# Kernel tuning notes

Measured on AMD Instinct MI355X. Metric: run time of the kernel, lower is better.

Reference implementation:

```python
import jax, jax.numpy as jnp
import numpy as np

D_IN = 4096
D_OUT = 4096
EPS_NORM = 1e-6
EPS_Q = 1e-8


def _ternary_quantize(w):
    # per-output-channel absmean scale, then round/clamp to {-1,0,1}
    gamma = jnp.mean(jnp.abs(w), axis=-1)
    w_q = jnp.clip(jnp.round(w / (gamma[:, None] + EPS_Q)), -1.0, 1.0)
    return w_q, gamma


def setup_inputs() -> dict:
    key = jax.random.key(0)
    kx, kw = jax.random.split(key)
    x = jax.random.normal(kx, (2, 4096, D_IN), dtype=jnp.float32)
    # kaiming-uniform-like init then ternarize (mirrors torch __init__)
    bound = 1.0 / np.sqrt(D_IN)
    w_init = jax.random.uniform(kw, (D_OUT, D_IN), minval=-bound, maxval=bound, dtype=jnp.float32)
    w_q, gamma = _ternary_quantize(w_init)
    norm_weight = jnp.ones((D_IN,), dtype=jnp.float32)
    return {"x": x, "norm_weight": norm_weight, "w_q": w_q, "gamma": gamma}


def reference(x, norm_weight, w_q, gamma):
    # RMSNorm
    rms = jnp.sqrt(jnp.mean(x * x, axis=-1, keepdims=True) + EPS_NORM)
    xn = x / rms * norm_weight
    # ternary linear (dense fp32 GEMM, math identical to F.linear) + per-channel scale
    y = jnp.einsum('bsd,od->bso', xn, w_q) * gamma
    return y
```

## Files before the change

### kernel.cpp

```cpp
#include <hip/hip_runtime.h>
#include <hip/hip_bf16.h>
#include <stdint.h>

#define D_IN  4096
#define D_OUT 4096
#define MROWS 8192

using i32x4 = __attribute__((ext_vector_type(4))) int;

__global__ __launch_bounds__(256) void prep_kernel(
    const float* __restrict__ x, const float* __restrict__ nw,
    signed char* __restrict__ xq, float* __restrict__ srow,
    const float* __restrict__ wq, signed char* __restrict__ wb) {
  const int b = blockIdx.x;
  const int t = threadIdx.x;

  if (b < 2048) {
    const int lane = t & 63;
    const int row  = b * 4 + (t >> 6);
    const float4* xr  = (const float4*)(x + (size_t)row * D_IN);
    const float4* nw4 = (const float4*)nw;

    float4 p[16];
    float ss = 0.f, mx = 0.f;
#pragma unroll
    for (int c = 0; c < 4; ++c) {
      float4 v[4], w[4];
#pragma unroll
      for (int i = 0; i < 4; ++i) {
        v[i] = xr[(c * 4 + i) * 64 + lane];
        w[i] = nw4[(c * 4 + i) * 64 + lane];
      }
#pragma unroll
      for (int i = 0; i < 4; ++i) {
        ss += v[i].x * v[i].x + v[i].y * v[i].y +
              v[i].z * v[i].z + v[i].w * v[i].w;
        float4 pp;
        pp.x = v[i].x * w[i].x; pp.y = v[i].y * w[i].y;
        pp.z = v[i].z * w[i].z; pp.w = v[i].w * w[i].w;
        p[c * 4 + i] = pp;
        mx = fmaxf(mx, fmaxf(fmaxf(fabsf(pp.x), fabsf(pp.y)),
                             fmaxf(fabsf(pp.z), fabsf(pp.w))));
      }
    }
#pragma unroll
    for (int off = 1; off < 64; off <<= 1) {
      ss += __shfl_xor(ss, off, 64);
      mx = fmaxf(mx, __shfl_xor(mx, off, 64));
    }
    const float scale  = rsqrtf(ss * (1.0f / D_IN) + 1e-6f);
    const float rowmax = mx * scale;
    const float s = fmaxf(rowmax, 1e-20f) * (1.0f / 127.0f);
    const float f = scale / s;
    if (lane == 0) srow[row] = s;

    int* out = (int*)(xq + (size_t)row * D_IN);
#pragma unroll
    for (int i = 0; i < 16; ++i) {
      const int q0 = (int)rintf(p[i].x * f);
      const int q1 = (int)rintf(p[i].y * f);
      const int q2 = (int)rintf(p[i].z * f);
      const int q3 = (int)rintf(p[i].w * f);
      out[i * 64 + lane] =
          (q0 & 0xFF) | ((q1 & 0xFF) << 8) | ((q2 & 0xFF) << 16) | (q3 << 24);
    }
  } else {
    const int cb = b - 2048;
    const float4* w4 = (const float4*)wq;
    int* o = (int*)wb;
#pragma unroll
    for (int i = 0; i < 4; ++i) {
      const int idx = cb * 1024 + i * 256 + t;
      const float4 v = w4[idx];
      const int q0 = (int)v.x, q1 = (int)v.y, q2 = (int)v.z, q3 = (int)v.w;
      o[idx] = (q0 & 0xFF) | ((q1 & 0xFF) << 8) | ((q2 & 0xFF) << 16) | (q3 << 24);
    }
  }
}

#define BM 256
#define BN 256
#define BKB 64
#define NKT (D_IN / BKB)
#define SLOT_BYTES (BM * BKB)

#define WVM(n_) asm volatile("s_waitcnt vmcnt(" #n_ ")" ::: "memory")
#define BAR()   __builtin_amdgcn_s_barrier()

#define STAGE(t_)                                                             \
  do {                                                                        \
    _Pragma("unroll") for (int _i = 0; _i < 2; ++_i)                          \
        __builtin_amdgcn_global_load_lds(                                     \
            (__attribute__((address_space(1))) void*)(A + aOff[_i] +          \
                                                      (t_) * BKB),            \
            (__attribute__((address_space(3))) void*)&sA[(t_) & 3]            \
                                                       [ldsOff[_i]],          \
            16, 0, 0);                                                        \
    _Pragma("unroll") for (int _i = 0; _i < 2; ++_i)                          \
        __builtin_amdgcn_global_load_lds(                                     \
            (__attribute__((address_space(1))) void*)(B + bOff[_i] +          \
                                                      (t_) * BKB),            \
            (__attribute__((address_space(3))) void*)&sB[(t_) & 3]            \
                                                       [ldsOff[_i]],          \
            16, 0, 0);                                                        \
  } while (0)

#define READF(t_, fa_, fb_)                                                   \
  do {                                                                        \
    _Pragma("unroll") for (int _i = 0; _i < 8; ++_i)                          \
        fa_[_i] = *(const i32x4*)&sA[(t_) & 3][aoff0 + _i * (16 * BKB)];      \
    _Pragma("unroll") for (int _j = 0; _j < 4; ++_j)                          \
        fb_[_j] = *(const i32x4*)&sB[(t_) & 3][boff0 + _j * (16 * BKB)];      \
  } while (0)

#define MFMA_C(fa_, fb_)                                                      \
  do {                                                                        \
    __builtin_amdgcn_s_setprio(1);                                            \
    _Pragma("unroll") for (int _i = 0; _i < 8; ++_i)                          \
        _Pragma("unroll") for (int _j = 0; _j < 4; ++_j)                      \
            acc[_i][_j] = __builtin_amdgcn_mfma_i32_16x16x64_i8(              \
                fa_[_i], fb_[_j], acc[_i][_j], 0, 0, 0);                      \
    __builtin_amdgcn_s_setprio(0);                                            \
  } while (0)

#define BODY_A(T_, fcA_, fcB_, fnA_, fnB_, STG_, WAIT_)                       \
  do {                                                                        \
    READF((T_) + 1, fnA_, fnB_);                                              \
    STG_;                                                                     \
    MFMA_C(fcA_, fcB_);                                                       \
    WAIT_;                                                                    \
    BAR();                                                                    \
  } while (0)

#define BODY_B(T_, fcA_, fcB_, fnA_, fnB_, STG_, WAIT_)                       \
  do {                                                                        \
    MFMA_C(fcA_, fcB_);                                                       \
    READF((T_) + 1, fnA_, fnB_);                                              \
    STG_;                                                                     \
    WAIT_;                                                                    \
    BAR();                                                                    \
  } while (0)

__global__ __launch_bounds__(512, 2) void gemm_kernel(
    const signed char* __restrict__ A,
    const signed char* __restrict__ B,
    const float* __restrict__ srow,
    const float* __restrict__ gamma,
    float* __restrict__ C) {
  __shared__ __align__(16) signed char sA[4][SLOT_BYTES];
  __shared__ __align__(16) signed char sB[4][SLOT_BYTES];

  const int tid  = threadIdx.x;
  const int lane = tid & 63;
  const int wv   = tid >> 6;
  const int wm   = wv >> 2;
  const int wn   = wv & 3;
  const int bn   = blockIdx.x;
  const int bm   = blockIdx.y;

  i32x4 acc[8][4];
#pragma unroll
  for (int i = 0; i < 8; ++i)
#pragma unroll
    for (int j = 0; j < 4; ++j) acc[i][j] = (i32x4){0, 0, 0, 0};

  size_t aOff[2], bOff[2];
  int ldsOff[2];
#pragma unroll
  for (int i = 0; i < 2; ++i) {
    const int c  = i * 512 + tid;
    const int r  = c >> 2;
    const int cc = ((c & 3) ^ ((r >> 1) & 3)) * 16;
    aOff[i] = (size_t)(bm * BM + r) * D_IN + cc;
    bOff[i] = (size_t)(bn * BN + r) * D_IN + cc;
    ldsOff[i] = (i * 512 + wv * 64) * 16;
  }

  const int kk    = (((lane >> 4) ^ ((lane >> 1) & 3))) * 16;
  const int aoff0 = (wm * 128 + (lane & 15)) * BKB + kk;
  const int boff0 = (wn * 64  + (lane & 15)) * BKB + kk;

  i32x4 f0a[8], f0b[4], f1a[8], f1b[4];

  STAGE(0); STAGE(1); STAGE(2);
  WVM(4);
  BAR();
  READF(0, f0a, f0b);

  if (wm) {
#pragma unroll 1
    for (int T = 0; T < NKT - 4; T += 2) {
      BODY_B(T,     f0a, f0b, f1a, f1b, STAGE(T + 3), WVM(4));
      BODY_B(T + 1, f1a, f1b, f0a, f0b, STAGE(T + 4), WVM(4));
    }
    BODY_B(60, f0a, f0b, f1a, f1b, STAGE(63), WVM(4));
    BODY_B(61, f1a, f1b, f0a, f0b, ,          WVM(0));
  } else {
#pragma unroll 1
    for (int T = 0; T < NKT - 4; T += 2) {
      BODY_A(T,     f0a, f0b, f1a, f1b, STAGE(T + 3), WVM(4));
      BODY_A(T + 1, f1a, f1b, f0a, f0b, STAGE(T + 4), WVM(4));
    }
    BODY_A(60, f0a, f0b, f1a, f1b, STAGE(63), WVM(4));
    BODY_A(61, f1a, f1b, f0a, f0b, ,          WVM(0));
  }
  READF(63, f1a, f1b);
  MFMA_C(f0a, f0b);
  MFMA_C(f1a, f1b);

  const int col0 = bn * BN + wn * 64 + (lane & 15);
  const int row0 = bm * BM + wm * 128 + ((lane >> 4) * 4);
  float g[4];
#pragma unroll
  for (int j = 0; j < 4; ++j) g[j] = gamma[col0 + j * 16];

#pragma unroll
  for (int i = 0; i < 8; ++i) {
#pragma unroll
    for (int r = 0; r < 4; ++r) {
      const int row = row0 + i * 16 + r;
      const float sr = srow[row];
#pragma unroll
      for (int j = 0; j < 4; ++j) {
        C[(size_t)row * D_OUT + col0 + j * 16] =
            (float)acc[i][j][r] * sr * g[j];
      }
    }
  }
}

#undef BODY_A
#undef BODY_B
#undef MFMA_C
#undef READF
#undef STAGE
#undef WVM
#undef BAR

extern "C" void kernel_launch(void* const* d_in, const int* in_sizes, int n_in,
                              void* d_out, int out_size, void* d_ws, size_t ws_size,
                              hipStream_t stream) {
  const float* x     = (const float*)d_in[0];
  const float* nw    = (const float*)d_in[1];
  const float* wq    = (const float*)d_in[2];
  const float* gamma = (const float*)d_in[3];
  float* y = (float*)d_out;

  signed char* xq = (signed char*)d_ws;
  signed char* wb = xq + (size_t)MROWS * D_IN;
  float* srow = (float*)(wb + (size_t)D_OUT * D_IN);

  prep_kernel<<<2048 + 4096, 256, 0, stream>>>(x, nw, xq, srow, wq, wb);

  gemm_kernel<<<dim3(D_OUT / BN, MROWS / BM), 512, 0, stream>>>(xq, wb, srow, gamma, y);
}
```

Before: 383.0 us.

## Shrink GEMM tile to 128x128 with 4 waves and drop split wave scheduling

Reduces the int8 GEMM block tile from 256x256 (8 waves) to 128x128 (4 waves, 64x64 per wave), cutting per-wave accumulators and fragments in half. It also removes the split where half the waves ran MFMA before LDS reads and half after, using a single read-then-compute ordering. The smaller tile gives 2048 blocks instead of 512, which may improve occupancy and tail balance. In exchange, global and LDS traffic per MFMA roughly doubles and the wave-staggered overlap is lost.

```diff
diff --git a/kernel.cpp b/kernel.cpp
--- a/kernel.cpp
+++ b/kernel.cpp
@@ -78,8 +78,8 @@
   }
 }
 
-#define BM 256
-#define BN 256
+#define BM 128
+#define BN 128
 #define BKB 64
 #define NKT (D_IN / BKB)
 #define SLOT_BYTES (BM * BKB)
@@ -107,7 +107,7 @@
 
 #define READF(t_, fa_, fb_)                                                   \
   do {                                                                        \
-    _Pragma("unroll") for (int _i = 0; _i < 8; ++_i)                          \
+    _Pragma("unroll") for (int _i = 0; _i < 4; ++_i)                          \
         fa_[_i] = *(const i32x4*)&sA[(t_) & 3][aoff0 + _i * (16 * BKB)];      \
     _Pragma("unroll") for (int _j = 0; _j < 4; ++_j)                          \
         fb_[_j] = *(const i32x4*)&sB[(t_) & 3][boff0 + _j * (16 * BKB)];      \
@@ -116,14 +116,14 @@
 #define MFMA_C(fa_, fb_)                                                      \
   do {                                                                        \
     __builtin_amdgcn_s_setprio(1);                                            \
-    _Pragma("unroll") for (int _i = 0; _i < 8; ++_i)                          \
+    _Pragma("unroll") for (int _i = 0; _i < 4; ++_i)                          \
         _Pragma("unroll") for (int _j = 0; _j < 4; ++_j)                      \
             acc[_i][_j] = __builtin_amdgcn_mfma_i32_16x16x64_i8(              \
                 fa_[_i], fb_[_j], acc[_i][_j], 0, 0, 0);                      \
     __builtin_amdgcn_s_setprio(0);                                            \
   } while (0)
 
-#define BODY_A(T_, fcA_, fcB_, fnA_, fnB_, STG_, WAIT_)                       \
+#define BODY(T_, fcA_, fcB_, fnA_, fnB_, STG_, WAIT_)                         \
   do {                                                                        \
     READF((T_) + 1, fnA_, fnB_);                                              \
     STG_;                                                                     \
@@ -132,16 +132,7 @@
     BAR();                                                                    \
   } while (0)
 
-#define BODY_B(T_, fcA_, fcB_, fnA_, fnB_, STG_, WAIT_)                       \
-  do {                                                                        \
-    MFMA_C(fcA_, fcB_);                                                       \
-    READF((T_) + 1, fnA_, fnB_);                                              \
-    STG_;                                                                     \
-    WAIT_;                                                                    \
-    BAR();                                                                    \
-  } while (0)
-
-__global__ __launch_bounds__(512, 2) void gemm_kernel(
+__global__ __launch_bounds__(256, 2) void gemm_kernel(
     const signed char* __restrict__ A,
     const signed char* __restrict__ B,
     const float* __restrict__ srow,
@@ -153,14 +144,14 @@
   const int tid  = threadIdx.x;
   const int lane = tid & 63;
   const int wv   = tid >> 6;
-  const int wm   = wv >> 2;
-  const int wn   = wv & 3;
+  const int wm   = wv >> 1;
+  const int wn   = wv & 1;
   const int bn   = blockIdx.x;
   const int bm   = blockIdx.y;
 
-  i32x4 acc[8][4];
-#pragma unroll
-  for (int i = 0; i < 8; ++i)
+  i32x4 acc[4][4];
+#pragma unroll
+  for (int i = 0; i < 4; ++i)
 #pragma unroll
     for (int j = 0; j < 4; ++j) acc[i][j] = (i32x4){0, 0, 0, 0};
 
@@ -168,54 +159,44 @@
   int ldsOff[2];
 #pragma unroll
   for (int i = 0; i < 2; ++i) {
-    const int c  = i * 512 + tid;
+    const int c  = i * 256 + tid;
     const int r  = c >> 2;
     const int cc = ((c & 3) ^ ((r >> 1) & 3)) * 16;
     aOff[i] = (size_t)(bm * BM + r) * D_IN + cc;
     bOff[i] = (size_t)(bn * BN + r) * D_IN + cc;
-    ldsOff[i] = (i * 512 + wv * 64) * 16;
+    ldsOff[i] = (i * 256 + wv * 64) * 16;
   }
 
   const int kk    = (((lane >> 4) ^ ((lane >> 1) & 3))) * 16;
-  const int aoff0 = (wm * 128 + (lane & 15)) * BKB + kk;
-  const int boff0 = (wn * 64  + (lane & 15)) * BKB + kk;
-
-  i32x4 f0a[8], f0b[4], f1a[8], f1b[4];
+  const int aoff0 = (wm * 64 + (lane & 15)) * BKB + kk;
+  const int boff0 = (wn * 64 + (lane & 15)) * BKB + kk;
+
+  i32x4 f0a[4], f0b[4], f1a[4], f1b[4];
 
   STAGE(0); STAGE(1); STAGE(2);
   WVM(4);
   BAR();
   READF(0, f0a, f0b);
 
-  if (wm) {
 #pragma unroll 1
-    for (int T = 0; T < NKT - 4; T += 2) {
-      BODY_B(T,     f0a, f0b, f1a, f1b, STAGE(T + 3), WVM(4));
-      BODY_B(T + 1, f1a, f1b, f0a, f0b, STAGE(T + 4), WVM(4));
-    }
-    BODY_B(60, f0a, f0b, f1a, f1b, STAGE(63), WVM(4));
-    BODY_B(61, f1a, f1b, f0a, f0b, ,          WVM(0));
-  } else {
-#pragma unroll 1
-    for (int T = 0; T < NKT - 4; T += 2) {
-      BODY_A(T,     f0a, f0b, f1a, f1b, STAGE(T + 3), WVM(4));
-      BODY_A(T + 1, f1a, f1b, f0a, f0b, STAGE(T + 4), WVM(4));
-    }
-    BODY_A(60, f0a, f0b, f1a, f1b, STAGE(63), WVM(4));
-    BODY_A(61, f1a, f1b, f0a, f0b, ,          WVM(0));
-  }
+  for (int T = 0; T < NKT - 4; T += 2) {
+    BODY(T,     f0a, f0b, f1a, f1b, STAGE(T + 3), WVM(4));
+    BODY(T + 1, f1a, f1b, f0a, f0b, STAGE(T + 4), WVM(4));
+  }
+  BODY(60, f0a, f0b, f1a, f1b, STAGE(63), WVM(4));
+  BODY(61, f1a, f1b, f0a, f0b, ,          WVM(0));
   READF(63, f1a, f1b);
   MFMA_C(f0a, f0b);
   MFMA_C(f1a, f1b);
 
   const int col0 = bn * BN + wn * 64 + (lane & 15);
-  const int row0 = bm * BM + wm * 128 + ((lane >> 4) * 4);
+  const int row0 = bm * BM + wm * 64 + ((lane >> 4) * 4);
   float g[4];
 #pragma unroll
   for (int j = 0; j < 4; ++j) g[j] = gamma[col0 + j * 16];
 
 #pragma unroll
-  for (int i = 0; i < 8; ++i) {
+  for (int i = 0; i < 4; ++i) {
 #pragma unroll
     for (int r = 0; r < 4; ++r) {
       const int row = row0 + i * 16 + r;
@@ -229,8 +210,7 @@
   }
 }
 
-#undef BODY_A
-#undef BODY_B
+#undef BODY
 #undef MFMA_C
 #undef READF
 #undef STAGE
@@ -252,5 +232,5 @@
 
   prep_kernel<<<2048 + 4096, 256, 0, stream>>>(x, nw, xq, srow, wq, wb);
 
-  gemm_kernel<<<dim3(D_OUT / BN, MROWS / BM), 512, 0, stream>>>(xq, wb, srow, gamma, y);
+  gemm_kernel<<<dim3(D_OUT / BN, MROWS / BM), 256, 0, stream>>>(xq, wb, srow, gamma, y);
 }
```

New measurement: 411.3 us. 7.4% more time.

## Pre-swizzle weights into MFMA fragment layout and load B directly to registers

Applied to the files above, without the earlier changes.

The weight packing step now writes int8 weights in a per-16-row tile, per-k-step fragment layout so each lane's MFMA B operand is one contiguous 16-byte chunk. The GEMM drops the LDS staging buffer for B and loads B fragments straight from global memory into registers one step ahead, keeping only A in LDS. This halves LDS use and LDS traffic and removes the split wave-scheduling variants, but B loads now go through the global/L2 path per wave without LDS sharing across waves, and the vmcnt waits were adjusted.

```diff
diff --git a/kernel.cpp b/kernel.cpp
--- a/kernel.cpp
+++ b/kernel.cpp
@@ -66,15 +66,24 @@
     }
   } else {
     const int cb = b - 2048;
-    const float4* w4 = (const float4*)wq;
-    int* o = (int*)wb;
+    const int c  = cb * 256 + t;
+    const int nt = c >> 12;
+    const int cc = c & 4095;
+    const int ks = cc >> 6;
+    const int l  = cc & 63;
+    const int row  = nt * 16 + (l & 15);
+    const int col0 = ks * 64 + (l >> 4) * 16;
+    const float4* src = (const float4*)(wq + (size_t)row * D_IN + col0);
+    int o4[4];
 #pragma unroll
     for (int i = 0; i < 4; ++i) {
-      const int idx = cb * 1024 + i * 256 + t;
-      const float4 v = w4[idx];
+      const float4 v = src[i];
       const int q0 = (int)v.x, q1 = (int)v.y, q2 = (int)v.z, q3 = (int)v.w;
-      o[idx] = (q0 & 0xFF) | ((q1 & 0xFF) << 8) | ((q2 & 0xFF) << 16) | (q3 << 24);
-    }
+      o4[i] = (q0 & 0xFF) | ((q1 & 0xFF) << 8) | ((q2 & 0xFF) << 16) |
+              (q3 << 24);
+    }
+    *(i32x4*)(wb + (size_t)nt * 65536 + ks * 1024 + l * 16) =
+        (i32x4){o4[0], o4[1], o4[2], o4[3]};
   }
 }
 
@@ -87,7 +96,7 @@
 #define WVM(n_) asm volatile("s_waitcnt vmcnt(" #n_ ")" ::: "memory")
 #define BAR()   __builtin_amdgcn_s_barrier()
 
-#define STAGE(t_)                                                             \
+#define STAGE_A(t_)                                                           \
   do {                                                                        \
     _Pragma("unroll") for (int _i = 0; _i < 2; ++_i)                          \
         __builtin_amdgcn_global_load_lds(                                     \
@@ -96,47 +105,36 @@
             (__attribute__((address_space(3))) void*)&sA[(t_) & 3]            \
                                                        [ldsOff[_i]],          \
             16, 0, 0);                                                        \
-    _Pragma("unroll") for (int _i = 0; _i < 2; ++_i)                          \
-        __builtin_amdgcn_global_load_lds(                                     \
-            (__attribute__((address_space(1))) void*)(B + bOff[_i] +          \
-                                                      (t_) * BKB),            \
-            (__attribute__((address_space(3))) void*)&sB[(t_) & 3]            \
-                                                       [ldsOff[_i]],          \
-            16, 0, 0);                                                        \
-  } while (0)
-
-#define READF(t_, fa_, fb_)                                                   \
+  } while (0)
+
+#define READF_A(t_, fa_)                                                      \
   do {                                                                        \
     _Pragma("unroll") for (int _i = 0; _i < 8; ++_i)                          \
         fa_[_i] = *(const i32x4*)&sA[(t_) & 3][aoff0 + _i * (16 * BKB)];      \
+  } while (0)
+
+#define LOADB(t_, bf_)                                                        \
+  do {                                                                        \
     _Pragma("unroll") for (int _j = 0; _j < 4; ++_j)                          \
-        fb_[_j] = *(const i32x4*)&sB[(t_) & 3][boff0 + _j * (16 * BKB)];      \
-  } while (0)
-
-#define MFMA_C(fa_, fb_)                                                      \
+        bf_[_j] = *(const i32x4*)(Bp[_j] + (size_t)(t_) * 1024);              \
+  } while (0)
+
+#define MFMA_C(fa_, bf_)                                                      \
   do {                                                                        \
     __builtin_amdgcn_s_setprio(1);                                            \
     _Pragma("unroll") for (int _i = 0; _i < 8; ++_i)                          \
         _Pragma("unroll") for (int _j = 0; _j < 4; ++_j)                      \
             acc[_i][_j] = __builtin_amdgcn_mfma_i32_16x16x64_i8(              \
-                fa_[_i], fb_[_j], acc[_i][_j], 0, 0, 0);                      \
+                fa_[_i], bf_[_j], acc[_i][_j], 0, 0, 0);                      \
     __builtin_amdgcn_s_setprio(0);                                            \
   } while (0)
 
-#define BODY_A(T_, fcA_, fcB_, fnA_, fnB_, STG_, WAIT_)                       \
-  do {                                                                        \
-    READF((T_) + 1, fnA_, fnB_);                                              \
+#define BODY(T_, fcA_, bfc_, fnA_, bfn_, STG_, WAIT_)                         \
+  do {                                                                        \
+    READF_A((T_) + 1, fnA_);                                                  \
+    LOADB((T_) + 1, bfn_);                                                    \
     STG_;                                                                     \
-    MFMA_C(fcA_, fcB_);                                                       \
-    WAIT_;                                                                    \
-    BAR();                                                                    \
-  } while (0)
-
-#define BODY_B(T_, fcA_, fcB_, fnA_, fnB_, STG_, WAIT_)                       \
-  do {                                                                        \
-    MFMA_C(fcA_, fcB_);                                                       \
-    READF((T_) + 1, fnA_, fnB_);                                              \
-    STG_;                                                                     \
+    MFMA_C(fcA_, bfc_);                                                       \
     WAIT_;                                                                    \
     BAR();                                                                    \
   } while (0)
@@ -148,7 +146,6 @@
     const float* __restrict__ gamma,
     float* __restrict__ C) {
   __shared__ __align__(16) signed char sA[4][SLOT_BYTES];
-  __shared__ __align__(16) signed char sB[4][SLOT_BYTES];
 
   const int tid  = threadIdx.x;
   const int lane = tid & 63;
@@ -164,7 +161,7 @@
 #pragma unroll
     for (int j = 0; j < 4; ++j) acc[i][j] = (i32x4){0, 0, 0, 0};
 
-  size_t aOff[2], bOff[2];
+  size_t aOff[2];
   int ldsOff[2];
 #pragma unroll
   for (int i = 0; i < 2; ++i) {
@@ -172,41 +169,36 @@
     const int r  = c >> 2;
     const int cc = ((c & 3) ^ ((r >> 1) & 3)) * 16;
     aOff[i] = (size_t)(bm * BM + r) * D_IN + cc;
-    bOff[i] = (size_t)(bn * BN + r) * D_IN + cc;
     ldsOff[i] = (i * 512 + wv * 64) * 16;
   }
 
   const int kk    = (((lane >> 4) ^ ((lane >> 1) & 3))) * 16;
   const int aoff0 = (wm * 128 + (lane & 15)) * BKB + kk;
-  const int boff0 = (wn * 64  + (lane & 15)) * BKB + kk;
-
-  i32x4 f0a[8], f0b[4], f1a[8], f1b[4];
-
-  STAGE(0); STAGE(1); STAGE(2);
-  WVM(4);
+
+  const signed char* Bp[4];
+#pragma unroll
+  for (int j = 0; j < 4; ++j)
+    Bp[j] = B + (size_t)(bn * 16 + wn * 4 + j) * 65536 + lane * 16;
+
+  i32x4 f0a[8], f1a[8], bf0[4], bf1[4];
+
+  STAGE_A(0); STAGE_A(1); STAGE_A(2);
+  LOADB(0, bf0);
+  WVM(6);
   BAR();
-  READF(0, f0a, f0b);
-
-  if (wm) {
+  READF_A(0, f0a);
+
 #pragma unroll 1
-    for (int T = 0; T < NKT - 4; T += 2) {
-      BODY_B(T,     f0a, f0b, f1a, f1b, STAGE(T + 3), WVM(4));
-      BODY_B(T + 1, f1a, f1b, f0a, f0b, STAGE(T + 4), WVM(4));
-    }
-    BODY_B(60, f0a, f0b, f1a, f1b, STAGE(63), WVM(4));
-    BODY_B(61, f1a, f1b, f0a, f0b, ,          WVM(0));
-  } else {
-#pragma unroll 1
-    for (int T = 0; T < NKT - 4; T += 2) {
-      BODY_A(T,     f0a, f0b, f1a, f1b, STAGE(T + 3), WVM(4));
-      BODY_A(T + 1, f1a, f1b, f0a, f0b, STAGE(T + 4), WVM(4));
-    }
-    BODY_A(60, f0a, f0b, f1a, f1b, STAGE(63), WVM(4));
-    BODY_A(61, f1a, f1b, f0a, f0b, ,          WVM(0));
-  }
-  READF(63, f1a, f1b);
-  MFMA_C(f0a, f0b);
-  MFMA_C(f1a, f1b);
+  for (int T = 0; T < NKT - 4; T += 2) {
+    BODY(T,     f0a, bf0, f1a, bf1, STAGE_A(T + 3), WVM(6));
+    BODY(T + 1, f1a, bf1, f0a, bf0, STAGE_A(T + 4), WVM(6));
+  }
+  BODY(60, f0a, bf0, f1a, bf1, STAGE_A(63), WVM(6));
+  BODY(61, f1a, bf1, f0a, bf0, ,            WVM(4));
+  READF_A(63, f1a);
+  LOADB(63, bf1);
+  MFMA_C(f0a, bf0);
+  MFMA_C(f1a, bf1);
 
   const int col0 = bn * BN + wn * 64 + (lane & 15);
   const int row0 = bm * BM + wm * 128 + ((lane >> 4) * 4);
@@ -229,11 +221,11 @@
   }
 }
 
-#undef BODY_A
-#undef BODY_B
+#undef BODY
 #undef MFMA_C
-#undef READF
-#undef STAGE
+#undef LOADB
+#undef READF_A
+#undef STAGE_A
 #undef WVM
 #undef BAR
 
```

New measurement: 393.1 us. +2.6%, slower.

## Swizzle block-to-tile mapping and unify wave pipeline ordering

Applied to the files above, without the earlier changes.

Remaps the linear block index so that consecutive blocks (likely spread across XCDs in groups of 8) take contiguous tiles. The goal is better L2 reuse of the A and B panels per chiplet. It also drops the split where half the waves ran MFMA-first and the other half ran LDS-read-first, so all waves now use one schedule that issues the next fragment reads before the MFMAs. This removes the deliberate staggering between wave groups, which may reduce overlap between LDS reads and MFMA issue. The hardcoded 16/64 constants assume the 16x32 grid.

```diff
diff --git a/kernel.cpp b/kernel.cpp
--- a/kernel.cpp
+++ b/kernel.cpp
@@ -123,20 +123,11 @@
     __builtin_amdgcn_s_setprio(0);                                            \
   } while (0)
 
-#define BODY_A(T_, fcA_, fcB_, fnA_, fnB_, STG_, WAIT_)                       \
+#define BODY(T_, fcA_, fcB_, fnA_, fnB_, STG_, WAIT_)                         \
   do {                                                                        \
     READF((T_) + 1, fnA_, fnB_);                                              \
     STG_;                                                                     \
     MFMA_C(fcA_, fcB_);                                                       \
-    WAIT_;                                                                    \
-    BAR();                                                                    \
-  } while (0)
-
-#define BODY_B(T_, fcA_, fcB_, fnA_, fnB_, STG_, WAIT_)                       \
-  do {                                                                        \
-    MFMA_C(fcA_, fcB_);                                                       \
-    READF((T_) + 1, fnA_, fnB_);                                              \
-    STG_;                                                                     \
     WAIT_;                                                                    \
     BAR();                                                                    \
   } while (0)
@@ -155,8 +146,11 @@
   const int wv   = tid >> 6;
   const int wm   = wv >> 2;
   const int wn   = wv & 3;
-  const int bn   = blockIdx.x;
-  const int bm   = blockIdx.y;
+
+  const int lin = blockIdx.x + blockIdx.y * (D_OUT / BN);
+  const int swz = (lin & 7) * 64 + (lin >> 3);
+  const int bn  = swz & 15;
+  const int bm  = swz >> 4;
 
   i32x4 acc[8][4];
 #pragma unroll
@@ -187,23 +181,13 @@
   BAR();
   READF(0, f0a, f0b);
 
-  if (wm) {
 #pragma unroll 1
-    for (int T = 0; T < NKT - 4; T += 2) {
-      BODY_B(T,     f0a, f0b, f1a, f1b, STAGE(T + 3), WVM(4));
-      BODY_B(T + 1, f1a, f1b, f0a, f0b, STAGE(T + 4), WVM(4));
-    }
-    BODY_B(60, f0a, f0b, f1a, f1b, STAGE(63), WVM(4));
-    BODY_B(61, f1a, f1b, f0a, f0b, ,          WVM(0));
-  } else {
-#pragma unroll 1
-    for (int T = 0; T < NKT - 4; T += 2) {
-      BODY_A(T,     f0a, f0b, f1a, f1b, STAGE(T + 3), WVM(4));
-      BODY_A(T + 1, f1a, f1b, f0a, f0b, STAGE(T + 4), WVM(4));
-    }
-    BODY_A(60, f0a, f0b, f1a, f1b, STAGE(63), WVM(4));
-    BODY_A(61, f1a, f1b, f0a, f0b, ,          WVM(0));
-  }
+  for (int T = 0; T < NKT - 4; T += 2) {
+    BODY(T,     f0a, f0b, f1a, f1b, STAGE(T + 3), WVM(4));
+    BODY(T + 1, f1a, f1b, f0a, f0b, STAGE(T + 4), WVM(4));
+  }
+  BODY(60, f0a, f0b, f1a, f1b, STAGE(63), WVM(4));
+  BODY(61, f1a, f1b, f0a, f0b, ,          WVM(0));
   READF(63, f1a, f1b);
   MFMA_C(f0a, f0b);
   MFMA_C(f1a, f1b);
@@ -229,8 +213,7 @@
   }
 }
 
-#undef BODY_A
-#undef BODY_B
+#undef BODY
 #undef MFMA_C
 #undef READF
 #undef STAGE
```

Result: no change. 385.2 us (+0.6%).
